# Kernel optimization log

Hardware: AMD Instinct MI355X
Metric: run time of the kernel (lower is better)

## Reference

```python
import jax, jax.numpy as jnp
import numpy as np

KSIZE = 5

def _sigmas(ksize, sigma_color, sigma_space):
    if sigma_space == 0:
        sigma_space = 0.15 * ksize + 0.35
    if sigma_color == 0:
        sigma_color = sigma_space
    return sigma_color, sigma_space

def _space_kernel(ksize, sigma):
    # matches getGaussianKernel (sigma > 0 branch)
    xs = jnp.arange(ksize, dtype=jnp.float32) - ksize // 2
    k1 = jnp.exp(-xs**2 / (2.0 * sigma * sigma))
    k2 = k1[:, None] * k1[None, :]
    return k2 / k2.sum()

def bilateral(x, ksize, sigma_color, sigma_space):
    sigma_color, sigma_space = _sigmas(ksize, sigma_color, sigma_space)
    pad = (ksize - 1) // 2
    B, C, H, W = x.shape
    xp = jnp.pad(x, ((0, 0), (0, 0), (pad, pad), (pad, pad)), mode='reflect')
    # patches[b,c,h,w,ki,kj] == padded[b,c,h+ki,w+kj] (same layout as torch unfold)
    patches = jnp.stack(
        [xp[:, :, i:i + H, j:j + W] for i in range(ksize) for j in range(ksize)],
        axis=-1,
    ).reshape(B, C, H, W, ksize, ksize)
    diff = patches - x[..., None, None]
    w_color = jnp.exp(-diff**2 / (2.0 * sigma_color * sigma_color))
    w_color = w_color / w_color.sum(axis=(-1, -2), keepdims=True)
    w_space = _space_kernel(ksize, sigma_space)  # [k,k], broadcasts
    w = w_color * w_space
    return (w * patches).sum(axis=(-1, -2)) / w.sum(axis=(-1, -2))

def setup_inputs() -> dict:
    key = jax.random.key(0)
    x = jax.random.uniform(key, (16, 3, 512, 512), dtype=jnp.float32)
    return {"x": x}

def reference(x):
    return bilateral(x, KSIZE, 0.0, 0.0)
```

## Files before the change

kernel.cpp:

```cpp
#include <hip/hip_runtime.h>


typedef float v2f __attribute__((ext_vector_type(2)));

constexpr int H_ = 512;
constexpr int W_ = 512;

__global__ __launch_bounds__(256, 4) void bilateral_kernel(
    const float* __restrict__ x,
    float* __restrict__ out,
    int nthreads)
{
    int t = blockIdx.x * 256 + threadIdx.x;
    if (t >= nthreads) return;

    int qx = t & 127;
    int rg = (t >> 7) & 127;
    int pl = t >> 14;
    int w0 = qx << 2;
    int h0 = rg << 2;
    const float* plane = x + ((long)pl << 18);
    float* oplane = out + ((long)pl << 18);

    int aL = max(w0 - 2, 0);
    int aR = min(w0 + 4, W_ - 2);
    bool bL = (w0 == 0);
    bool bR = (w0 == W_ - 4);

    float Wn[8][8];
#pragma unroll
    for (int k = 0; k < 8; ++k) {
        int r = h0 + k - 2;
        r = min(abs(r), 2 * (H_ - 1) - r);
        const float* rp = plane + r * W_;
        float2 l2 = *(const float2*)(rp + aL);
        float4 c4 = *(const float4*)(rp + w0);
        float2 r2 = *(const float2*)(rp + aR);
        Wn[k][2] = c4.x; Wn[k][3] = c4.y; Wn[k][4] = c4.z; Wn[k][5] = c4.w;
        Wn[k][0] = bL ? c4.z : l2.x;
        Wn[k][1] = l2.y;
        Wn[k][6] = r2.x;
        Wn[k][7] = bR ? c4.y : r2.y;
    }

#pragma unroll
    for (int k = 0; k < 8; ++k)
#pragma unroll
        for (int j = 0; j < 8; ++j)
            asm volatile("" : "+v"(Wn[k][j]));

    const float coef2 = -0.59615498f;
    const v2f k2 = {coef2, coef2};

#pragma unroll
    for (int oi = 0; oi < 4; ++oi) {
        v2f numA = {0.f, 0.f}, denA = {0.f, 0.f};
        v2f numB = {0.f, 0.f}, denB = {0.f, 0.f};
        v2f cA = {Wn[oi + 2][2], Wn[oi + 2][3]};
        v2f cB = {Wn[oi + 2][4], Wn[oi + 2][5]};
#pragma unroll
        for (int di = 0; di < 5; ++di) {
#pragma unroll
            for (int dj = 0; dj < 5; ++dj) {
                float csf = coef2 * (float)((di - 2) * (di - 2) +
                                            (dj - 2) * (dj - 2));
                v2f cs = {csf, csf};
                v2f pA = {Wn[oi + di][dj],     Wn[oi + di][dj + 1]};
                v2f pB = {Wn[oi + di][dj + 2], Wn[oi + di][dj + 3]};
                v2f dA = pA - cA;
                v2f dB = pB - cB;
                v2f argA = (dA * k2) * dA + cs;
                v2f argB = (dB * k2) * dB + cs;
                v2f wA, wB;
                wA.x = __builtin_amdgcn_exp2f(argA.x);
                wA.y = __builtin_amdgcn_exp2f(argA.y);
                wB.x = __builtin_amdgcn_exp2f(argB.x);
                wB.y = __builtin_amdgcn_exp2f(argB.y);
                numA += wA * pA;
                denA += wA;
                numB += wB * pB;
                denB += wB;
            }
        }
        float4 o;
        o.x = numA.x * __builtin_amdgcn_rcpf(denA.x);
        o.y = numA.y * __builtin_amdgcn_rcpf(denA.y);
        o.z = numB.x * __builtin_amdgcn_rcpf(denB.x);
        o.w = numB.y * __builtin_amdgcn_rcpf(denB.y);
        *(float4*)(oplane + (h0 + oi) * W_ + w0) = o;
    }
}

extern "C" void kernel_launch(void* const* d_in, const int* in_sizes, int n_in,
                              void* d_out, int out_size, void* d_ws, size_t ws_size,
                              hipStream_t stream)
{
    const float* x = (const float*)d_in[0];
    float* out = (float*)d_out;
    int nthreads = in_sizes[0] >> 4;
    int blocks = (nthreads + 255) / 256;
    bilateral_kernel<<<blocks, 256, 0, stream>>>(x, out, nthreads);
}
```

Measured before the change: 124.4 us.

## Stage 64x64 image tiles with halo in LDS before bilateral compute

Each block now loads a 64x64 output tile plus reflect-padded halo into shared memory with scalar coalesced loads, then each thread reads its 8x8 window from LDS instead of issuing strided global vector loads per thread. The aim is to cut redundant global/L2 traffic from overlapping halos and the reflect-boundary selects. It adds a __syncthreads, about 20 KB of LDS per block that can limit occupancy, and scalar global loads. The register-pinning asm barrier is also removed.

```diff
diff --git a/kernel.cpp b/kernel.cpp
--- a/kernel.cpp
+++ b/kernel.cpp
@@ -1,53 +1,59 @@
 #include <hip/hip_runtime.h>
 
 
-typedef float v2f __attribute__((ext_vector_type(2)));
-
 constexpr int H_ = 512;
 constexpr int W_ = 512;
+constexpr int TSTRIDE = 74;
+constexpr int TROWS = 68;
+constexpr int TCOLS = 72;
+
+typedef float v2f __attribute__((ext_vector_type(2)));
 
 __global__ __launch_bounds__(256, 4) void bilateral_kernel(
     const float* __restrict__ x,
-    float* __restrict__ out,
-    int nthreads)
+    float* __restrict__ out)
 {
-    int t = blockIdx.x * 256 + threadIdx.x;
-    if (t >= nthreads) return;
+    __shared__ float lds[TROWS * TSTRIDE];
 
-    int qx = t & 127;
-    int rg = (t >> 7) & 127;
-    int pl = t >> 14;
-    int w0 = qx << 2;
-    int h0 = rg << 2;
+    int tid = threadIdx.x;
+    int blk = blockIdx.x;
+    int pl  = blk >> 6;
+    int bi  = blk & 63;
+    int w0b = (bi & 7) << 6;
+    int h0b = (bi >> 3) << 6;
+
     const float* plane = x + ((long)pl << 18);
     float* oplane = out + ((long)pl << 18);
 
-    int aL = max(w0 - 2, 0);
-    int aR = min(w0 + 4, W_ - 2);
-    bool bL = (w0 == 0);
-    bool bR = (w0 == W_ - 4);
+#pragma unroll
+    for (int k = 0; k < 20; ++k) {
+        int f = k * 256 + tid;
+        if (f < TROWS * TCOLS) {
+            int row = (unsigned)f / TCOLS;
+            int col = f - row * TCOLS;
+            int gr = h0b + row - 2;
+            gr = min(abs(gr), 2 * (H_ - 1) - gr);
+            int gc = w0b + col - 4;
+            gc = min(abs(gc), 2 * (W_ - 1) - gc);
+            lds[row * TSTRIDE + col] = plane[gr * W_ + gc];
+        }
+    }
+    __syncthreads();
+
+    int tx = tid & 15, ty = tid >> 4;
+    const float* wbase = lds + (ty * 4) * TSTRIDE + tx * 4 + 2;
 
     float Wn[8][8];
 #pragma unroll
     for (int k = 0; k < 8; ++k) {
-        int r = h0 + k - 2;
-        r = min(abs(r), 2 * (H_ - 1) - r);
-        const float* rp = plane + r * W_;
-        float2 l2 = *(const float2*)(rp + aL);
-        float4 c4 = *(const float4*)(rp + w0);
-        float2 r2 = *(const float2*)(rp + aR);
-        Wn[k][2] = c4.x; Wn[k][3] = c4.y; Wn[k][4] = c4.z; Wn[k][5] = c4.w;
-        Wn[k][0] = bL ? c4.z : l2.x;
-        Wn[k][1] = l2.y;
-        Wn[k][6] = r2.x;
-        Wn[k][7] = bR ? c4.y : r2.y;
+        const float* rp = wbase + k * TSTRIDE;
+#pragma unroll
+        for (int j = 0; j < 8; j += 2) {
+            float2 v = *(const float2*)(rp + j);
+            Wn[k][j] = v.x;
+            Wn[k][j + 1] = v.y;
+        }
     }
-
-#pragma unroll
-    for (int k = 0; k < 8; ++k)
-#pragma unroll
-        for (int j = 0; j < 8; ++j)
-            asm volatile("" : "+v"(Wn[k][j]));
 
     const float coef2 = -0.59615498f;
     const v2f k2 = {coef2, coef2};
@@ -87,7 +93,7 @@
         o.y = numA.y * __builtin_amdgcn_rcpf(denA.y);
         o.z = numB.x * __builtin_amdgcn_rcpf(denB.x);
         o.w = numB.y * __builtin_amdgcn_rcpf(denB.y);
-        *(float4*)(oplane + (h0 + oi) * W_ + w0) = o;
+        *(float4*)(oplane + (h0b + ty * 4 + oi) * W_ + w0b + tx * 4) = o;
     }
 }
 
@@ -97,7 +103,6 @@
 {
     const float* x = (const float*)d_in[0];
     float* out = (float*)d_out;
-    int nthreads = in_sizes[0] >> 4;
-    int blocks = (nthreads + 255) / 256;
-    bilateral_kernel<<<blocks, 256, 0, stream>>>(x, out, nthreads);
+    int nblocks = (in_sizes[0] >> 18) * 64;
+    bilateral_kernel<<<nblocks, 256, 0, stream>>>(x, out);
 }
```

New measurement: 136.1 us. 1.09x slower.
